# Kernel optimization log

Measured on AMD Instinct MI355X. Metric: run time of the kernel, lower is better.

## Reference

```python
import jax, jax.numpy as jnp
import numpy as np

EPS = 1e-12  # F.normalize default eps


def _l2norm(x):
    n = jnp.linalg.norm(x, axis=-1, keepdims=True)
    return x / jnp.maximum(n, EPS)


def _group_pool(x):
    # x: (b, 4, C) row-normalized features; per-group attention pooling.
    # s_i = sum_j x_i . x_j ; weights = softmax_i(s) ; pooled = sum_i w_i x_i
    s = jnp.einsum('bic,bjc->bi', x, x)          # (b, 4)
    w = jax.nn.softmax(s, axis=1)                 # (b, 4)
    return jnp.einsum('bi,bic->bc', w, x)         # (b, C)


def setup_inputs() -> dict:
    key = jax.random.key(0)
    k1, k2 = jax.random.split(key)
    N, C = 16384, 1024
    x1 = jax.random.normal(k1, (N, C), dtype=jnp.float32)
    x2 = jax.random.normal(k2, (N, C), dtype=jnp.float32)
    return {"x1": x1, "x2": x2}


def reference(x1, x2):
    b = x2.shape[0] // 4
    C = x1.shape[1]
    x1n = _l2norm(x1).reshape(b, 4, C)
    x2n = _l2norm(x2).reshape(b, 4, C)
    p1 = _l2norm(_group_pool(x1n))                # (b, C)
    p2 = _l2norm(_group_pool(x2n))                # (b, C)
    center_loss = jnp.mean(jnp.linalg.norm(p1 - p2, axis=1))
    sim = p1 @ p2.T                               # (b, b)
    diag = jnp.arange(b)
    # cross_entropy(sim, arange) and cross_entropy(sim.T, arange)
    loss_t = -jnp.mean(jax.nn.log_softmax(sim, axis=1)[diag, diag])
    loss_i = -jnp.mean(jax.nn.log_softmax(sim, axis=0)[diag, diag])
    return (loss_t + loss_i + center_loss, p1, p2)
```

## Files before the change

### kernel.cpp

```cpp
#include <hip/hip_runtime.h>
#include <hip/hip_bf16.h>

#define BGRP 4096
#define CDIM 1024

typedef __attribute__((ext_vector_type(8))) short bf16x8;
typedef __attribute__((ext_vector_type(4))) float f32x4;
typedef __attribute__((ext_vector_type(4))) unsigned short u16x4;

__device__ __forceinline__ unsigned short f2bf(float x) {
    __hip_bfloat16 h = __float2bfloat16(x);
    unsigned short u;
    __builtin_memcpy(&u, &h, 2);
    return u;
}

__device__ __forceinline__ void gload16(const void* g, void* l) {
    __builtin_amdgcn_global_load_lds(
        (const __attribute__((address_space(1))) unsigned int*)g,
        (__attribute__((address_space(3))) unsigned int*)l, 16, 0, 0);
}

template<int NV>
__device__ __forceinline__ void block_reduce(float* vals, float* lds) {
    const int lane = threadIdx.x & 63;
    const int wid  = threadIdx.x >> 6;
    #pragma unroll
    for (int v = 0; v < NV; ++v) {
        float x = vals[v];
        #pragma unroll
        for (int off = 32; off > 0; off >>= 1) x += __shfl_down(x, off, 64);
        if (lane == 0) lds[v * 4 + wid] = x;
    }
    __syncthreads();
    #pragma unroll
    for (int v = 0; v < NV; ++v)
        vals[v] = lds[v * 4 + 0] + lds[v * 4 + 1] + lds[v * 4 + 2] + lds[v * 4 + 3];
    __syncthreads();
}

__device__ __forceinline__ void group_coefs(const float* d, float* coef) {
    float D[4][4];
    int c = 0;
    #pragma unroll
    for (int i = 0; i < 4; ++i)
        #pragma unroll
        for (int j = i; j < 4; ++j) { D[i][j] = d[c]; D[j][i] = d[c]; ++c; }
    float inv[4];
    #pragma unroll
    for (int i = 0; i < 4; ++i) inv[i] = 1.0f / fmaxf(sqrtf(D[i][i]), 1e-12f);
    float s[4];
    #pragma unroll
    for (int i = 0; i < 4; ++i) {
        float si = 0.f;
        #pragma unroll
        for (int j = 0; j < 4; ++j) si += D[i][j] * inv[i] * inv[j];
        s[i] = si;
    }
    float m = fmaxf(fmaxf(s[0], s[1]), fmaxf(s[2], s[3]));
    float e[4], se = 0.f;
    #pragma unroll
    for (int i = 0; i < 4; ++i) { e[i] = expf(s[i] - m); se += e[i]; }
    float rse = 1.0f / se;
    #pragma unroll
    for (int i = 0; i < 4; ++i) coef[i] = e[i] * rse * inv[i];
}

__global__ __launch_bounds__(256) void pool_kernel(
    const float* __restrict__ x1, const float* __restrict__ x2,
    float* __restrict__ out,
    unsigned short* __restrict__ p1b, unsigned short* __restrict__ p2b,
    float* __restrict__ diag, float* __restrict__ centerArr)
{
    __shared__ float lds[80];
    const int g = blockIdx.x;
    const int t = threadIdx.x;

    float a1[4][4], a2[4][4];
    #pragma unroll
    for (int i = 0; i < 4; ++i) {
        float4 v1 = reinterpret_cast<const float4*>(x1)[(size_t)(4 * g + i) * 256 + t];
        float4 v2 = reinterpret_cast<const float4*>(x2)[(size_t)(4 * g + i) * 256 + t];
        a1[i][0] = v1.x; a1[i][1] = v1.y; a1[i][2] = v1.z; a1[i][3] = v1.w;
        a2[i][0] = v2.x; a2[i][1] = v2.y; a2[i][2] = v2.z; a2[i][3] = v2.w;
    }

    float red[20];
    {
        int c = 0;
        #pragma unroll
        for (int i = 0; i < 4; ++i)
            #pragma unroll
            for (int j = i; j < 4; ++j) {
                float s1 = 0.f, s2 = 0.f;
                #pragma unroll
                for (int e = 0; e < 4; ++e) {
                    s1 += a1[i][e] * a1[j][e];
                    s2 += a2[i][e] * a2[j][e];
                }
                red[c] = s1; red[10 + c] = s2;
                ++c;
            }
    }
    block_reduce<20>(red, lds);

    float c1[4], c2[4];
    group_coefs(red, c1);
    group_coefs(red + 10, c2);

    float q1[4], q2[4];
    #pragma unroll
    for (int e = 0; e < 4; ++e) {
        float s1 = 0.f, s2 = 0.f;
        #pragma unroll
        for (int i = 0; i < 4; ++i) { s1 += c1[i] * a1[i][e]; s2 += c2[i] * a2[i][e]; }
        q1[e] = s1; q2[e] = s2;
    }

    float red2[3];
    red2[0] = q1[0]*q1[0] + q1[1]*q1[1] + q1[2]*q1[2] + q1[3]*q1[3];
    red2[1] = q2[0]*q2[0] + q2[1]*q2[1] + q2[2]*q2[2] + q2[3]*q2[3];
    red2[2] = q1[0]*q2[0] + q1[1]*q2[1] + q1[2]*q2[2] + q1[3]*q2[3];
    block_reduce<3>(red2, lds);
    const float n1 = red2[0], n2 = red2[1], d12 = red2[2];
    const float i1 = 1.0f / fmaxf(sqrtf(n1), 1e-12f);
    const float i2 = 1.0f / fmaxf(sqrtf(n2), 1e-12f);

    float p1v[4], p2v[4];
    #pragma unroll
    for (int e = 0; e < 4; ++e) { p1v[e] = q1[e] * i1; p2v[e] = q2[e] * i2; }

    float* p1o = out + 1 + (size_t)g * CDIM + t * 4;
    float* p2o = p1o + (size_t)BGRP * CDIM;
    #pragma unroll
    for (int e = 0; e < 4; ++e) { p1o[e] = p1v[e]; p2o[e] = p2v[e]; }

    if (p1b != nullptr) {
        u16x4 w1, w2;
        #pragma unroll
        for (int e = 0; e < 4; ++e) { w1[e] = f2bf(p1v[e]); w2[e] = f2bf(p2v[e]); }
        *reinterpret_cast<u16x4*>(p1b + (size_t)g * CDIM + t * 4) = w1;
        *reinterpret_cast<u16x4*>(p2b + (size_t)g * CDIM + t * 4) = w2;
    }

    if (t == 0) {
        const float dg = i1 * i2 * d12;
        diag[g] = dg;
        const float c2v = fmaxf(n1 * i1 * i1 + n2 * i2 * i2 - 2.0f * dg, 0.0f);
        centerArr[g] = sqrtf(c2v);
    }
}

__global__ __launch_bounds__(256, 4) void sim_lds_kernel(
    const unsigned short* __restrict__ p1b, const unsigned short* __restrict__ p2b,
    float* __restrict__ rowsum, float* __restrict__ colsum)
{
    __shared__ __align__(16) unsigned char lds[32768];
    const int tid  = threadIdx.x;
    const int lane = tid & 63;
    const int wid  = tid >> 6;
    const int wm = wid >> 1, wn = wid & 1;
    const int row0 = blockIdx.y * 128;
    const int col0 = blockIdx.x * 128;
    const int lr  = lane & 15;
    const int lkb = lane >> 4;

    const int srow = lane >> 3;
    const int scol = ((lane & 7) ^ srow) << 4;
    const int ch0  = wid * 4;

    f32x4 acc[4][4];
    #pragma unroll
    for (int mi = 0; mi < 4; ++mi)
        #pragma unroll
        for (int ni = 0; ni < 4; ++ni) {
            acc[mi][ni][0] = 0.f; acc[mi][ni][1] = 0.f;
            acc[mi][ni][2] = 0.f; acc[mi][ni][3] = 0.f;
        }

    const char* A = (const char*)p1b;
    const char* B = (const char*)p2b;

    for (int kt = 0; kt < 16; ++kt) {
        const size_t kbyte = (size_t)kt * 128;
        #pragma unroll
        for (int c = 0; c < 4; ++c) {
            const int chunk = ch0 + c;
            const int r = chunk * 8 + srow;
            gload16(A + (size_t)(row0 + r) * 2048 + kbyte + scol, lds + chunk * 1024);
            gload16(B + (size_t)(col0 + r) * 2048 + kbyte + scol, lds + 16384 + chunk * 1024);
        }
        __syncthreads();

        #pragma unroll
        for (int ks = 0; ks < 2; ++ks) {
            bf16x8 af[4], bg[4];
            const int cbase = (ks * 64 + lkb * 16) ^ ((lr & 7) << 4);
            #pragma unroll
            for (int i = 0; i < 4; ++i) {
                const int ra = wm * 64 + i * 16 + lr;
                const int rb = wn * 64 + i * 16 + lr;
                af[i] = *reinterpret_cast<const bf16x8*>(lds + ra * 128 + cbase);
                bg[i] = *reinterpret_cast<const bf16x8*>(lds + 16384 + rb * 128 + cbase);
            }
            #pragma unroll
            for (int mi = 0; mi < 4; ++mi)
                #pragma unroll
                for (int ni = 0; ni < 4; ++ni)
                    acc[mi][ni] = __builtin_amdgcn_mfma_f32_16x16x32_bf16(
                        af[mi], bg[ni], acc[mi][ni], 0, 0, 0);
        }
        __syncthreads();
    }

    float rs[4][4];
    float cs[4] = {0.f, 0.f, 0.f, 0.f};
    #pragma unroll
    for (int mi = 0; mi < 4; ++mi)
        #pragma unroll
        for (int r = 0; r < 4; ++r) rs[mi][r] = 0.f;

    #pragma unroll
    for (int mi = 0; mi < 4; ++mi)
        #pragma unroll
        for (int ni = 0; ni < 4; ++ni)
            #pragma unroll
            for (int r = 0; r < 4; ++r) {
                float e = __expf(acc[mi][ni][r]);
                rs[mi][r] += e;
                cs[ni] += e;
            }

    const int wrow0 = row0 + wm * 64;
    const int wcol0 = col0 + wn * 64;
    #pragma unroll
    for (int mi = 0; mi < 4; ++mi)
        #pragma unroll
        for (int r = 0; r < 4; ++r) {
            float v = rs[mi][r];
            v += __shfl_xor(v, 1, 64);
            v += __shfl_xor(v, 2, 64);
            v += __shfl_xor(v, 4, 64);
            v += __shfl_xor(v, 8, 64);
            if (lr == 0) atomicAdd(&rowsum[wrow0 + mi * 16 + lkb * 4 + r], v);
        }
    #pragma unroll
    for (int ni = 0; ni < 4; ++ni) {
        float v = cs[ni];
        v += __shfl_xor(v, 16, 64);
        v += __shfl_xor(v, 32, 64);
        if (lkb == 0) atomicAdd(&colsum[wcol0 + ni * 16 + lr], v);
    }
}

__device__ __forceinline__ bf16x8 frag_from_f32(const float* p) {
    bf16x8 r;
    #pragma unroll
    for (int i = 0; i < 8; ++i) {
        unsigned int b = __float_as_uint(p[i]);
        b += 0x7fffu + ((b >> 16) & 1u);
        r[i] = (short)(b >> 16);
    }
    return r;
}

__global__ __launch_bounds__(256) void sim_fallback_kernel(
    const float* __restrict__ p1f, const float* __restrict__ p2f,
    float* __restrict__ rowsum, float* __restrict__ colsum)
{
    const int lane = threadIdx.x & 63;
    const int wid  = threadIdx.x >> 6;
    const int wm = wid >> 1, wn = wid & 1;
    const int row0 = blockIdx.y * 128 + wm * 64;
    const int col0 = blockIdx.x * 128 + wn * 64;
    const int lr  = lane & 15;
    const int lkb = lane >> 4;
    const int lk  = lkb * 8;

    f32x4 acc[4][4];
    #pragma unroll
    for (int mi = 0; mi < 4; ++mi)
        #pragma unroll
        for (int ni = 0; ni < 4; ++ni) {
            acc[mi][ni][0] = 0.f; acc[mi][ni][1] = 0.f;
            acc[mi][ni][2] = 0.f; acc[mi][ni][3] = 0.f;
        }

    const size_t abase = (size_t)(row0 + lr) * CDIM + lk;
    const size_t bbase = (size_t)(col0 + lr) * CDIM + lk;

    for (int k = 0; k < CDIM; k += 32) {
        bf16x8 af[4], bfr[4];
        #pragma unroll
        for (int i = 0; i < 4; ++i) {
            af[i]  = frag_from_f32(p1f + abase + (size_t)i * 16 * CDIM + k);
            bfr[i] = frag_from_f32(p2f + bbase + (size_t)i * 16 * CDIM + k);
        }
        #pragma unroll
        for (int mi = 0; mi < 4; ++mi)
            #pragma unroll
            for (int ni = 0; ni < 4; ++ni)
                acc[mi][ni] = __builtin_amdgcn_mfma_f32_16x16x32_bf16(
                    af[mi], bfr[ni], acc[mi][ni], 0, 0, 0);
    }

    float rs[4][4];
    float cs[4] = {0.f, 0.f, 0.f, 0.f};
    #pragma unroll
    for (int mi = 0; mi < 4; ++mi)
        #pragma unroll
        for (int r = 0; r < 4; ++r) rs[mi][r] = 0.f;

    #pragma unroll
    for (int mi = 0; mi < 4; ++mi)
        #pragma unroll
        for (int ni = 0; ni < 4; ++ni)
            #pragma unroll
            for (int r = 0; r < 4; ++r) {
                float e = __expf(acc[mi][ni][r]);
                rs[mi][r] += e;
                cs[ni] += e;
            }

    #pragma unroll
    for (int mi = 0; mi < 4; ++mi)
        #pragma unroll
        for (int r = 0; r < 4; ++r) {
            float v = rs[mi][r];
            v += __shfl_xor(v, 1, 64);
            v += __shfl_xor(v, 2, 64);
            v += __shfl_xor(v, 4, 64);
            v += __shfl_xor(v, 8, 64);
            if (lr == 0) atomicAdd(&rowsum[row0 + mi * 16 + lkb * 4 + r], v);
        }
    #pragma unroll
    for (int ni = 0; ni < 4; ++ni) {
        float v = cs[ni];
        v += __shfl_xor(v, 16, 64);
        v += __shfl_xor(v, 32, 64);
        if (lkb == 0) atomicAdd(&colsum[col0 + ni * 16 + lr], v);
    }
}

__global__ __launch_bounds__(256) void loss_kernel(
    const float* __restrict__ rowsum, const float* __restrict__ colsum,
    const float* __restrict__ diag, const float* __restrict__ centerArr,
    float* __restrict__ out)
{
    float part = 0.f;
    for (int i = threadIdx.x; i < BGRP; i += 256)
        part += logf(rowsum[i]) + logf(colsum[i]) - 2.0f * diag[i] + centerArr[i];
    #pragma unroll
    for (int off = 32; off > 0; off >>= 1) part += __shfl_down(part, off, 64);
    __shared__ float l4[4];
    if ((threadIdx.x & 63) == 0) l4[threadIdx.x >> 6] = part;
    __syncthreads();
    if (threadIdx.x == 0)
        out[0] = (l4[0] + l4[1] + l4[2] + l4[3]) * (1.0f / (float)BGRP);
}

extern "C" void kernel_launch(void* const* d_in, const int* in_sizes, int n_in,
                              void* d_out, int out_size, void* d_ws, size_t ws_size,
                              hipStream_t stream)
{
    const float* x1 = (const float*)d_in[0];
    const float* x2 = (const float*)d_in[1];
    float* out = (float*)d_out;

    float* rowsum    = (float*)d_ws;
    float* colsum    = rowsum + BGRP;
    float* diag      = colsum + BGRP;
    float* centerArr = diag + BGRP;
    const size_t head_floats = 4 * (size_t)BGRP;
    unsigned short* p1b = (unsigned short*)((char*)d_ws + head_floats * sizeof(float));
    unsigned short* p2b = p1b + (size_t)BGRP * CDIM;
    const size_t need = head_floats * sizeof(float) + (size_t)2 * BGRP * CDIM * sizeof(unsigned short);
    const bool use_ws = (ws_size >= need);

    hipMemsetAsync(d_ws, 0, 2 * (size_t)BGRP * sizeof(float), stream);

    pool_kernel<<<BGRP, 256, 0, stream>>>(x1, x2, out,
                                          use_ws ? p1b : nullptr,
                                          use_ws ? p2b : nullptr,
                                          diag, centerArr);

    dim3 gridB(BGRP / 128, BGRP / 128);
    if (use_ws) {
        sim_lds_kernel<<<gridB, 256, 0, stream>>>(p1b, p2b, rowsum, colsum);
    } else {
        sim_fallback_kernel<<<gridB, 256, 0, stream>>>(out + 1, out + 1 + (size_t)BGRP * CDIM,
                                                       rowsum, colsum);
    }

    loss_kernel<<<1, 256, 0, stream>>>(rowsum, colsum, diag, centerArr, out);
}
```

Baseline: 98.50 us.

## Assign one wavefront per group in pool kernel to drop block reductions

The pool kernel now maps each 64-lane wavefront to one group of four rows instead of a full 256-thread block per group. All dot-product reductions become wave-level xor shuffles, so the LDS staging and __syncthreads barriers go away. The pooled norm is computed algebraically from the Gram matrix and coefficients rather than by a second reduction. The trade-off is 16 float4 registers per input per thread and x1/x2 processed sequentially, with launch bounds set to 3 blocks per SIMD.

```diff
diff --git a/kernel.cpp b/kernel.cpp
--- a/kernel.cpp
+++ b/kernel.cpp
@@ -21,24 +21,6 @@
         (__attribute__((address_space(3))) unsigned int*)l, 16, 0, 0);
 }
 
-template<int NV>
-__device__ __forceinline__ void block_reduce(float* vals, float* lds) {
-    const int lane = threadIdx.x & 63;
-    const int wid  = threadIdx.x >> 6;
-    #pragma unroll
-    for (int v = 0; v < NV; ++v) {
-        float x = vals[v];
-        #pragma unroll
-        for (int off = 32; off > 0; off >>= 1) x += __shfl_down(x, off, 64);
-        if (lane == 0) lds[v * 4 + wid] = x;
-    }
-    __syncthreads();
-    #pragma unroll
-    for (int v = 0; v < NV; ++v)
-        vals[v] = lds[v * 4 + 0] + lds[v * 4 + 1] + lds[v * 4 + 2] + lds[v * 4 + 3];
-    __syncthreads();
-}
-
 __device__ __forceinline__ void group_coefs(const float* d, float* coef) {
     float D[4][4];
     int c = 0;
@@ -66,87 +48,115 @@
     for (int i = 0; i < 4; ++i) coef[i] = e[i] * rse * inv[i];
 }
 
-__global__ __launch_bounds__(256) void pool_kernel(
+__device__ __forceinline__ float wave_allsum(float t) {
+    t += __shfl_xor(t, 1, 64);
+    t += __shfl_xor(t, 2, 64);
+    t += __shfl_xor(t, 4, 64);
+    t += __shfl_xor(t, 8, 64);
+    t += __shfl_xor(t, 16, 64);
+    t += __shfl_xor(t, 32, 64);
+    return t;
+}
+
+__device__ __forceinline__ void pool_phase(
+    const float* __restrict__ x, int g, int l,
+    float* __restrict__ pout,
+    unsigned short* __restrict__ pbout,
+    float4 p[4], float& s_out)
+{
+    float4 a[4][4];
+    #pragma unroll
+    for (int i = 0; i < 4; ++i)
+        #pragma unroll
+        for (int w = 0; w < 4; ++w)
+            a[i][w] = reinterpret_cast<const float4*>(x)[(size_t)(4 * g + i) * 256 + w * 64 + l];
+
+    float dd[10];
+    {
+        int c = 0;
+        #pragma unroll
+        for (int i = 0; i < 4; ++i)
+            #pragma unroll
+            for (int j = i; j < 4; ++j) {
+                float s0 = 0.f;
+                #pragma unroll
+                for (int w = 0; w < 4; ++w)
+                    s0 += a[i][w].x * a[j][w].x + a[i][w].y * a[j][w].y
+                        + a[i][w].z * a[j][w].z + a[i][w].w * a[j][w].w;
+                dd[c++] = s0;
+            }
+    }
+    #pragma unroll
+    for (int v = 0; v < 10; ++v) dd[v] = wave_allsum(dd[v]);
+
+    float coef[4];
+    group_coefs(dd, coef);
+
+    float D[4][4];
+    {
+        int c = 0;
+        #pragma unroll
+        for (int i = 0; i < 4; ++i)
+            #pragma unroll
+            for (int j = i; j < 4; ++j) { D[i][j] = dd[c]; D[j][i] = dd[c]; ++c; }
+    }
+    float n = 0.f;
+    #pragma unroll
+    for (int i = 0; i < 4; ++i) {
+        float ti = 0.f;
+        #pragma unroll
+        for (int j = 0; j < 4; ++j) ti += D[i][j] * coef[j];
+        n += coef[i] * ti;
+    }
+    const float inv = 1.0f / fmaxf(sqrtf(n), 1e-12f);
+    s_out = n * inv * inv;
+
+    #pragma unroll
+    for (int w = 0; w < 4; ++w) {
+        float4 q;
+        q.x = coef[0]*a[0][w].x + coef[1]*a[1][w].x + coef[2]*a[2][w].x + coef[3]*a[3][w].x;
+        q.y = coef[0]*a[0][w].y + coef[1]*a[1][w].y + coef[2]*a[2][w].y + coef[3]*a[3][w].y;
+        q.z = coef[0]*a[0][w].z + coef[1]*a[1][w].z + coef[2]*a[2][w].z + coef[3]*a[3][w].z;
+        q.w = coef[0]*a[0][w].w + coef[1]*a[1][w].w + coef[2]*a[2][w].w + coef[3]*a[3][w].w;
+        q.x *= inv; q.y *= inv; q.z *= inv; q.w *= inv;
+        p[w] = q;
+
+        const int e = w * 256 + l * 4;
+        pout[e + 0] = q.x; pout[e + 1] = q.y; pout[e + 2] = q.z; pout[e + 3] = q.w;
+        if (pbout != nullptr) {
+            u16x4 wb;
+            wb[0] = f2bf(q.x); wb[1] = f2bf(q.y); wb[2] = f2bf(q.z); wb[3] = f2bf(q.w);
+            *reinterpret_cast<u16x4*>(pbout + e) = wb;
+        }
+    }
+}
+
+__global__ __launch_bounds__(256, 3) void pool_kernel(
     const float* __restrict__ x1, const float* __restrict__ x2,
     float* __restrict__ out,
     unsigned short* __restrict__ p1b, unsigned short* __restrict__ p2b,
     float* __restrict__ diag, float* __restrict__ centerArr)
 {
-    __shared__ float lds[80];
-    const int g = blockIdx.x;
-    const int t = threadIdx.x;
-
-    float a1[4][4], a2[4][4];
-    #pragma unroll
-    for (int i = 0; i < 4; ++i) {
-        float4 v1 = reinterpret_cast<const float4*>(x1)[(size_t)(4 * g + i) * 256 + t];
-        float4 v2 = reinterpret_cast<const float4*>(x2)[(size_t)(4 * g + i) * 256 + t];
-        a1[i][0] = v1.x; a1[i][1] = v1.y; a1[i][2] = v1.z; a1[i][3] = v1.w;
-        a2[i][0] = v2.x; a2[i][1] = v2.y; a2[i][2] = v2.z; a2[i][3] = v2.w;
-    }
-
-    float red[20];
-    {
-        int c = 0;
-        #pragma unroll
-        for (int i = 0; i < 4; ++i)
-            #pragma unroll
-            for (int j = i; j < 4; ++j) {
-                float s1 = 0.f, s2 = 0.f;
-                #pragma unroll
-                for (int e = 0; e < 4; ++e) {
-                    s1 += a1[i][e] * a1[j][e];
-                    s2 += a2[i][e] * a2[j][e];
-                }
-                red[c] = s1; red[10 + c] = s2;
-                ++c;
-            }
-    }
-    block_reduce<20>(red, lds);
-
-    float c1[4], c2[4];
-    group_coefs(red, c1);
-    group_coefs(red + 10, c2);
-
-    float q1[4], q2[4];
-    #pragma unroll
-    for (int e = 0; e < 4; ++e) {
-        float s1 = 0.f, s2 = 0.f;
-        #pragma unroll
-        for (int i = 0; i < 4; ++i) { s1 += c1[i] * a1[i][e]; s2 += c2[i] * a2[i][e]; }
-        q1[e] = s1; q2[e] = s2;
-    }
-
-    float red2[3];
-    red2[0] = q1[0]*q1[0] + q1[1]*q1[1] + q1[2]*q1[2] + q1[3]*q1[3];
-    red2[1] = q2[0]*q2[0] + q2[1]*q2[1] + q2[2]*q2[2] + q2[3]*q2[3];
-    red2[2] = q1[0]*q2[0] + q1[1]*q2[1] + q1[2]*q2[2] + q1[3]*q2[3];
-    block_reduce<3>(red2, lds);
-    const float n1 = red2[0], n2 = red2[1], d12 = red2[2];
-    const float i1 = 1.0f / fmaxf(sqrtf(n1), 1e-12f);
-    const float i2 = 1.0f / fmaxf(sqrtf(n2), 1e-12f);
-
-    float p1v[4], p2v[4];
-    #pragma unroll
-    for (int e = 0; e < 4; ++e) { p1v[e] = q1[e] * i1; p2v[e] = q2[e] * i2; }
-
-    float* p1o = out + 1 + (size_t)g * CDIM + t * 4;
-    float* p2o = p1o + (size_t)BGRP * CDIM;
-    #pragma unroll
-    for (int e = 0; e < 4; ++e) { p1o[e] = p1v[e]; p2o[e] = p2v[e]; }
-
-    if (p1b != nullptr) {
-        u16x4 w1, w2;
-        #pragma unroll
-        for (int e = 0; e < 4; ++e) { w1[e] = f2bf(p1v[e]); w2[e] = f2bf(p2v[e]); }
-        *reinterpret_cast<u16x4*>(p1b + (size_t)g * CDIM + t * 4) = w1;
-        *reinterpret_cast<u16x4*>(p2b + (size_t)g * CDIM + t * 4) = w2;
-    }
-
-    if (t == 0) {
-        const float dg = i1 * i2 * d12;
-        diag[g] = dg;
-        const float c2v = fmaxf(n1 * i1 * i1 + n2 * i2 * i2 - 2.0f * dg, 0.0f);
+    const int l = threadIdx.x & 63;
+    const int g = blockIdx.x * 4 + (threadIdx.x >> 6);
+
+    float4 p1s[4], p2s[4];
+    float s1, s2;
+    pool_phase(x1, g, l, out + 1 + (size_t)g * CDIM,
+               p1b ? p1b + (size_t)g * CDIM : nullptr, p1s, s1);
+    pool_phase(x2, g, l, out + 1 + (size_t)(BGRP + g) * CDIM,
+               p2b ? p2b + (size_t)g * CDIM : nullptr, p2s, s2);
+
+    float dp = 0.f;
+    #pragma unroll
+    for (int w = 0; w < 4; ++w)
+        dp += p1s[w].x * p2s[w].x + p1s[w].y * p2s[w].y
+            + p1s[w].z * p2s[w].z + p1s[w].w * p2s[w].w;
+    dp = wave_allsum(dp);
+
+    if (l == 0) {
+        diag[g] = dp;
+        const float c2v = fmaxf(s1 + s2 - 2.0f * dp, 0.0f);
         centerArr[g] = sqrtf(c2v);
     }
 }
@@ -379,10 +389,10 @@
 
     hipMemsetAsync(d_ws, 0, 2 * (size_t)BGRP * sizeof(float), stream);
 
-    pool_kernel<<<BGRP, 256, 0, stream>>>(x1, x2, out,
-                                          use_ws ? p1b : nullptr,
-                                          use_ws ? p2b : nullptr,
-                                          diag, centerArr);
+    pool_kernel<<<BGRP / 4, 256, 0, stream>>>(x1, x2, out,
+                                              use_ws ? p1b : nullptr,
+                                              use_ws ? p2b : nullptr,
+                                              diag, centerArr);
 
     dim3 gridB(BGRP / 128, BGRP / 128);
     if (use_ws) {
```

After: 87.27 us. 11.4% less time.
